# Optimization experiments

Measured on AMD Instinct MI355X. Metric: run time of the kernel, lower is better.

Reference implementation:

```python
import jax, jax.numpy as jnp
import numpy as np

B, T, E, H = 16, 4096, 64, 8
K, GADD, RADD, REGION = 256, 8, 8, 64
MIN_SIGMA, SIGMA_SCALE, SIGMA_BOOST = 0.05, 1.0, 2.0
VS = K * (4 + GADD + RADD)


def setup_inputs() -> dict:
    key = jax.random.key(0)
    ks = jax.random.split(key, 10)
    return {
        "x": jax.random.normal(ks[0], (B, T, E), jnp.float32),
        "Wq": jax.random.normal(ks[1], (E, E * H), jnp.float32) / np.float32(np.sqrt(E)),
        "Wk": jax.random.normal(ks[2], (E, E * H), jnp.float32) / np.float32(np.sqrt(E)),
        "Wv": jax.random.normal(ks[3], (E, E * H), jnp.float32) / np.float32(np.sqrt(E)),
        "Wu": jax.random.normal(ks[4], (H * E, E), jnp.float32) / np.float32(np.sqrt(H * E)),
        "bu": jnp.zeros((E,), jnp.float32),
        "means_p": jax.random.normal(ks[5], (K, 2), jnp.float32),
        "sigmas_p": jax.random.normal(ks[6], (K,), jnp.float32),
        "global_ints": jax.random.randint(ks[7], (B, 1, K, GADD, 2), 0, T, jnp.int32),
        "local_offsets": jax.random.randint(ks[8], (B, 1, K, RADD, 2), 0, REGION, jnp.int32),
    }


def _flip(x):
    # util.flip: sort each (i, j) pair so row >= col (below-diagonal / causal)
    hi = jnp.max(x, axis=-1, keepdims=True)
    lo = jnp.min(x, axis=-1, keepdims=True)
    return jnp.concatenate([hi, lo], axis=-1)


def _forward(x, Wq, Wk, Wv, Wu, bu, means_p, sigmas_p, global_ints, local_offsets):
    b, t, e = x.shape
    h, k = H, K

    # ---- hyper(): continuous means/sigmas over the (t, t) attention matrix
    means = jnp.broadcast_to(means_p[None, None], (b, 1, k, 2))
    means = _flip(means)
    means = jax.nn.sigmoid(means) * (t - 1)                       # (b,1,k,2) in [0, t-1]
    sig = jax.nn.softplus(sigmas_p + SIGMA_BOOST) + MIN_SIGMA     # (k,)
    sigmas = jnp.broadcast_to((sig * t * SIGMA_SCALE)[None, None, :, None], (b, 1, k, 2))

    # ---- ngenerate: 2^rank floor/ceil neighbours + global + relative-window samples
    fl, ce = jnp.floor(means), jnp.ceil(means)
    pat = jnp.array([[0., 0.], [0., 1.], [1., 0.], [1., 1.]], jnp.float32)  # (4,2)
    neigh = fl[:, :, :, None, :] * (1.0 - pat) + ce[:, :, :, None, :] * pat
    neigh = jnp.clip(neigh, 0, t - 1).astype(jnp.int32)           # (b,1,k,4,2)
    lower = jnp.clip(jnp.floor(means) - REGION // 2, 0, t - REGION).astype(jnp.int32)
    local = lower[:, :, :, None, :] + local_offsets               # (b,1,k,RADD,2)
    idx = jnp.concatenate([neigh, global_ints, local], axis=3).reshape(b, 1, VS, 2)
    idx = _flip(idx)                                              # (b,1,VS,2), row >= col

    # ---- densities: unnormalized Gaussian weight of each int tuple under each point
    indfl = idx.astype(jnp.float32)
    diff = (indfl[:, :, :, None, :] - means[:, :, None, :, :]) / sigmas[:, :, None, :, :]
    props = jnp.exp(-0.5 * jnp.sum(diff * diff, axis=-1))         # (b,1,VS,K)

    # ---- nduplicates: zero all-but-one of identical index tuples per batch
    ids = idx[:, 0, :, 0] * t + idx[:, 0, :, 1]                   # (b, VS)
    def dupmask(v):
        o = jnp.argsort(v)
        s = v[o]
        d = jnp.concatenate([jnp.zeros((1,), bool), s[1:] == s[:-1]])
        return jnp.zeros((VS,), bool).at[o].set(d)
    dups = jax.vmap(dupmask)(ids)                                  # (b, VS)
    props = jnp.where(dups[:, None, :, None], 0.0, props)
    props = props / jnp.sum(props, axis=2, keepdims=True)
    weights = jnp.sum(props, axis=3)                               # mvalues == 1 -> (b,1,VS)

    # ---- Q/K/V projections, per-head dim = e
    scale = e ** -0.25
    q = (x @ Wq).reshape(b, t, h, e).transpose(0, 2, 1, 3).reshape(b * h, t, e) * scale
    kk = (x @ Wk).reshape(b, t, h, e).transpose(0, 2, 1, 3).reshape(b * h, t, e) * scale
    v = (x @ Wv).reshape(b, t, h, e).transpose(0, 2, 1, 3).reshape(b * h, t, e)

    rows = jnp.broadcast_to(idx[:, 0, None, :, 0], (b, h, VS)).reshape(b * h, VS)
    cols = jnp.broadcast_to(idx[:, 0, None, :, 1], (b, h, VS)).reshape(b * h, VS)
    w = jnp.broadcast_to(weights[:, 0, None, :], (b, h, VS)).reshape(b * h, VS)

    sq = jnp.take_along_axis(q, rows[:, :, None], axis=1)          # (b*h, VS, e)
    sk = jnp.take_along_axis(kk, cols[:, :, None], axis=1)
    dot = w * jnp.sum(sq * sk, axis=-1)                            # (b*h, VS)

    # ---- segment (row-wise) softmax over the sparse pattern
    seg = (jnp.arange(b * h, dtype=jnp.int32)[:, None] * t + rows).reshape(-1)
    dflat = dot.reshape(-1)
    m = jax.lax.stop_gradient(jax.ops.segment_max(dflat, seg, num_segments=b * h * t))
    ex = jnp.exp(dflat - m[seg])
    ssum = jax.ops.segment_sum(ex, seg, num_segments=b * h * t)
    p = ex / ssum[seg]                                             # (b*h*VS,)

    # ---- sparse batched matmul: scatter-add p * V[col] into rows
    gathered = jnp.take_along_axis(v, cols[:, :, None], axis=1).reshape(-1, e)
    out = jax.ops.segment_sum(p[:, None] * gathered, seg, num_segments=b * h * t)
    out = out.reshape(b, h, t, e).transpose(0, 2, 1, 3).reshape(b, t, h * e)
    return out @ Wu + bu


def reference(x, Wq, Wk, Wv, Wu, bu, means_p, sigmas_p, global_ints, local_offsets):
    return _forward(x, Wq, Wk, Wv, Wu, bu, means_p, sigmas_p, global_ints, local_offsets)
```

## Files before the change

### kernel.cpp

```cpp
#include <hip/hip_runtime.h>
#include <hip/hip_bf16.h>
#include <math.h>

#define B 16
#define T 4096
#define E 64
#define H 8
#define KP 256
#define GADD 8
#define RADD 8
#define REGION 64
#define VS (KP * (4 + GADD + RADD))
#define NH (H * E)
#define NCHUNK 20
#define HSZ 16384

typedef __attribute__((ext_vector_type(8))) short bf16x8;
typedef __attribute__((ext_vector_type(4))) float f32x4;

__device__ inline ushort f2bf(float f) {
    union { __hip_bfloat16 h; ushort u; } cv;
    cv.h = __float2bfloat16(f);
    return cv.u;
}
__device__ inline float bflo(uint32_t p) { return __uint_as_float(p << 16); }
__device__ inline float bfhi(uint32_t p) { return __uint_as_float(p & 0xffff0000u); }
__device__ inline float sigm(float v) { return 1.f / (1.f + expf(-v)); }

__global__ void k_init(int* __restrict__ hkey, int* __restrict__ hval, int* __restrict__ chist) {
    int i = blockIdx.x * 256 + threadIdx.x;
    hkey[i] = -1;
    hval[i] = 0x7fffffff;
    #pragma unroll
    for (int j = 0; j < 5; ++j) chist[i + j * (B * HSZ)] = 0;
}

__global__ void k_prep_w(const float* __restrict__ Wq, const float* __restrict__ Wk,
                         const float* __restrict__ Wv, const float* __restrict__ Wu,
                         ushort* __restrict__ wfrag) {
    int t = blockIdx.x * 256 + threadIdx.x;
    if (t >= 3 * 32 * 2 * 64) return;
    int lane = t & 63, kf = (t >> 6) & 1, nf = (t >> 7) & 31, z = t >> 12;
    int col = nf * 16 + (lane & 15);
    int krow = kf * 32 + (lane >> 4) * 8;
    uint32_t v[8];
    if (z < 2) {
        const float* W = (z == 0) ? Wq : Wk;
        #pragma unroll
        for (int j = 0; j < 8; ++j) v[j] = f2bf(W[(size_t)(krow + j) * NH + col]);
    } else {
        int h = col >> 6, jc = col & 63;
        #pragma unroll
        for (int j = 0; j < 8; ++j) {
            const float* wvrow = Wv + (size_t)(krow + j) * NH + h * 64;
            const float* wucol = Wu + (size_t)h * 64 * 64 + jc;
            float acc = 0.f;
            for (int d = 0; d < 64; ++d) acc += wvrow[d] * wucol[d * 64];
            v[j] = f2bf(acc);
        }
    }
    uint4 r;
    r.x = v[0] | (v[1] << 16); r.y = v[2] | (v[3] << 16);
    r.z = v[4] | (v[5] << 16); r.w = v[6] | (v[7] << 16);
    *(uint4*)(wfrag + (size_t)t * 8) = r;
}

__global__ __launch_bounds__(256) void k_proj(const float* __restrict__ x,
        const ushort* __restrict__ wfrag,
        __hip_bfloat16* __restrict__ q, __hip_bfloat16* __restrict__ kk,
        __hip_bfloat16* __restrict__ vu) {
    int z = blockIdx.y;
    __hip_bfloat16* outp = (z == 0) ? q : (z == 1) ? kk : vu;
    int row0 = blockIdx.x * 64;
    int wv = threadIdx.x >> 6, lane = threadIdx.x & 63;
    int arow = lane & 15, akoff = (lane >> 4) * 8;

    bf16x8 bfr[8][2];
    #pragma unroll
    for (int nf = 0; nf < 8; ++nf) {
        size_t base = ((size_t)((z * 32 + wv * 8 + nf) * 2) * 64 + lane) * 8;
        bfr[nf][0] = *(const bf16x8*)(wfrag + base);
        bfr[nf][1] = *(const bf16x8*)(wfrag + base + 64 * 8);
    }

    #pragma unroll
    for (int mf = 0; mf < 4; ++mf) {
        const float* xp = x + (size_t)(row0 + mf * 16 + arow) * 64 + akoff;
        float4 fa0 = *(const float4*)xp;
        float4 fa1 = *(const float4*)(xp + 4);
        float4 fb0 = *(const float4*)(xp + 32);
        float4 fb1 = *(const float4*)(xp + 36);
        union { bf16x8 v; uint32_t u[4]; } ca, cb;
        ca.u[0] = (uint32_t)f2bf(fa0.x) | ((uint32_t)f2bf(fa0.y) << 16);
        ca.u[1] = (uint32_t)f2bf(fa0.z) | ((uint32_t)f2bf(fa0.w) << 16);
        ca.u[2] = (uint32_t)f2bf(fa1.x) | ((uint32_t)f2bf(fa1.y) << 16);
        ca.u[3] = (uint32_t)f2bf(fa1.z) | ((uint32_t)f2bf(fa1.w) << 16);
        cb.u[0] = (uint32_t)f2bf(fb0.x) | ((uint32_t)f2bf(fb0.y) << 16);
        cb.u[1] = (uint32_t)f2bf(fb0.z) | ((uint32_t)f2bf(fb0.w) << 16);
        cb.u[2] = (uint32_t)f2bf(fb1.x) | ((uint32_t)f2bf(fb1.y) << 16);
        cb.u[3] = (uint32_t)f2bf(fb1.z) | ((uint32_t)f2bf(fb1.w) << 16);
        bf16x8 a0 = ca.v, a1 = cb.v;
        f32x4 acc[8];
        #pragma unroll
        for (int nf = 0; nf < 8; ++nf) {
            f32x4 t = {0.f, 0.f, 0.f, 0.f};
            t = __builtin_amdgcn_mfma_f32_16x16x32_bf16(a0, bfr[nf][0], t, 0, 0, 0);
            t = __builtin_amdgcn_mfma_f32_16x16x32_bf16(a1, bfr[nf][1], t, 0, 0, 0);
            acc[nf] = t;
        }
        int rbase = row0 + mf * 16 + (lane >> 4) * 4;
        #pragma unroll
        for (int rg = 0; rg < 4; ++rg) {
            uint4 o;
            o.x = (uint32_t)f2bf(acc[0][rg]) | ((uint32_t)f2bf(acc[1][rg]) << 16);
            o.y = (uint32_t)f2bf(acc[2][rg]) | ((uint32_t)f2bf(acc[3][rg]) << 16);
            o.z = (uint32_t)f2bf(acc[4][rg]) | ((uint32_t)f2bf(acc[5][rg]) << 16);
            o.w = (uint32_t)f2bf(acc[6][rg]) | ((uint32_t)f2bf(acc[7][rg]) << 16);
            *(uint4*)((ushort*)outp + (size_t)(rbase + rg) * NH + wv * 128 + (lane & 15) * 8) = o;
        }
    }
}

__global__ void k_build_idx(const int* __restrict__ g_ints, const int* __restrict__ l_offs,
                            const float* __restrict__ means_p,
                            int* __restrict__ idxrow, int* __restrict__ idxcol,
                            int* __restrict__ hkey, int* __restrict__ hval) {
    int b = blockIdx.y;
    int s = blockIdx.x * 256 + threadIdx.x;
    int* keys = hkey + b * HSZ;
    int* vals = hval + b * HSZ;
    int k = s / 20, slot = s % 20;
    float pa = means_p[2 * k], pb = means_p[2 * k + 1];
    float m0 = sigm(fmaxf(pa, pb)) * (float)(T - 1);
    float m1 = sigm(fminf(pa, pb)) * (float)(T - 1);
    int i0, i1;
    if (slot < 4) {
        float a  = (slot & 2) ? ceilf(m0) : floorf(m0);
        float bb = (slot & 1) ? ceilf(m1) : floorf(m1);
        a  = fminf(fmaxf(a, 0.f), (float)(T - 1));
        bb = fminf(fmaxf(bb, 0.f), (float)(T - 1));
        i0 = (int)a; i1 = (int)bb;
    } else if (slot < 12) {
        const int* p = g_ints + ((size_t)((b * KP + k) * GADD) + (slot - 4)) * 2;
        i0 = p[0]; i1 = p[1];
    } else {
        int lo0 = (int)fminf(fmaxf(floorf(m0) - (float)(REGION / 2), 0.f), (float)(T - REGION));
        int lo1 = (int)fminf(fmaxf(floorf(m1) - (float)(REGION / 2), 0.f), (float)(T - REGION));
        const int* p = l_offs + ((size_t)((b * KP + k) * RADD) + (slot - 12)) * 2;
        i0 = lo0 + p[0]; i1 = lo1 + p[1];
    }
    int row = max(i0, i1), col = min(i0, i1);
    idxrow[b * VS + s] = row;
    idxcol[b * VS + s] = col;
    int id = row * T + col;
    unsigned h = ((unsigned)id * 2654435761u) >> 18;
    while (true) {
        int old = atomicCAS(&keys[h], -1, id);
        if (old == -1 || old == id) { atomicMin(&vals[h], s); break; }
        h = (h + 1) & (HSZ - 1);
    }
}

__global__ __launch_bounds__(256) void k_local(const int* __restrict__ idxrow,
        const int* __restrict__ idxcol, const int* __restrict__ hkey,
        const int* __restrict__ hval, int* __restrict__ lrank, int* __restrict__ dup,
        int* __restrict__ chist) {
    int b = blockIdx.y, chunk = blockIdx.x;
    int tid = threadIdx.x;
    int s = chunk * 256 + tid;
    int r = idxrow[b * VS + s];
    int c = idxcol[b * VS + s];
    __shared__ int srow[256];
    srow[tid] = r;
    __syncthreads();
    int lr = 0;
    #pragma unroll 8
    for (int t = 0; t < 256; ++t) {
        int rt = srow[t];
        lr += (t < tid && rt == r);
    }
    lrank[b * VS + s] = lr;
    atomicAdd(&chist[(size_t)(b * T + r) * NCHUNK + chunk], 1);
    const int* keys = hkey + b * HSZ;
    const int* vals = hval + b * HSZ;
    int id = r * T + c;
    unsigned h = ((unsigned)id * 2654435761u) >> 18;
    while (keys[h] != id) h = (h + 1) & (HSZ - 1);
    dup[b * VS + s] = (vals[h] != s);
}

__global__ void k_colsum(const int* __restrict__ idxrow, const int* __restrict__ idxcol,
                         const int* __restrict__ dup, const float* __restrict__ means_p,
                         const float* __restrict__ sigmas_p, float* __restrict__ colsum) {
    int k = blockIdx.x, b = blockIdx.y;
    float pa = means_p[2 * k], pb = means_p[2 * k + 1];
    float m0 = sigm(fmaxf(pa, pb)) * (float)(T - 1);
    float m1 = sigm(fminf(pa, pb)) * (float)(T - 1);
    float sp = sigmas_p[k] + 2.0f;
    float sg = (sp > 20.f) ? sp : log1pf(expf(sp));
    float inv = 1.f / ((sg + 0.05f) * (float)T);
    float acc = 0.f;
    for (int s = threadIdx.x; s < VS; s += 256) {
        if (!dup[b * VS + s]) {
            float d0 = ((float)idxrow[b * VS + s] - m0) * inv;
            float d1 = ((float)idxcol[b * VS + s] - m1) * inv;
            acc += __expf(-0.5f * (d0 * d0 + d1 * d1));
        }
    }
    __shared__ float red[256];
    red[threadIdx.x] = acc;
    __syncthreads();
    for (int o = 128; o > 0; o >>= 1) {
        if (threadIdx.x < o) red[threadIdx.x] += red[threadIdx.x + o];
        __syncthreads();
    }
    if (threadIdx.x == 0) colsum[b * KP + k] = red[0];
}

__global__ void k_weights(const int* __restrict__ idxrow, const int* __restrict__ idxcol,
                          const int* __restrict__ dup, const float* __restrict__ means_p,
                          const float* __restrict__ sigmas_p, const float* __restrict__ colsum,
                          float* __restrict__ wts) {
    int b = blockIdx.y;
    int s = blockIdx.x * 256 + threadIdx.x;
    __shared__ float sm[2 * KP], ss[KP], rc[KP];
    {
        int k = threadIdx.x;
        float pa = means_p[2 * k], pb = means_p[2 * k + 1];
        sm[2 * k]     = sigm(fmaxf(pa, pb)) * (float)(T - 1);
        sm[2 * k + 1] = sigm(fminf(pa, pb)) * (float)(T - 1);
        float sp = sigmas_p[k] + 2.0f;
        float sg = (sp > 20.f) ? sp : log1pf(expf(sp));
        ss[k] = 1.f / ((sg + 0.05f) * (float)T);
        rc[k] = 1.f / colsum[b * KP + k];
    }
    __syncthreads();
    float w = 0.f;
    if (!dup[b * VS + s]) {
        float r = (float)idxrow[b * VS + s], c = (float)idxcol[b * VS + s];
        #pragma unroll 4
        for (int k = 0; k < KP; ++k) {
            float d0 = (r - sm[2 * k]) * ss[k];
            float d1 = (c - sm[2 * k + 1]) * ss[k];
            w += __expf(-0.5f * (d0 * d0 + d1 * d1)) * rc[k];
        }
    }
    wts[b * VS + s] = w;
}

__global__ __launch_bounds__(1024) void k_scan(int* __restrict__ chist, int* __restrict__ rowptr) {
    int b = blockIdx.x, tid = threadIdx.x;
    __shared__ int part[1024];
    int v[4]; int loc = 0;
    #pragma unroll
    for (int j = 0; j < 4; ++j) {
        int row = tid * 4 + j;
        int* p = chist + (size_t)(b * T + row) * NCHUNK;
        int acc = 0;
        #pragma unroll
        for (int c = 0; c < NCHUNK; ++c) { int t = p[c]; p[c] = acc; acc += t; }
        v[j] = acc; loc += acc;
    }
    part[tid] = loc;
    __syncthreads();
    for (int off = 1; off < 1024; off <<= 1) {
        int t = (tid >= off) ? part[tid - off] : 0;
        __syncthreads();
        part[tid] += t;
        __syncthreads();
    }
    int excl = part[tid] - loc;
    #pragma unroll
    for (int j = 0; j < 4; ++j) { rowptr[b * (T + 1) + tid * 4 + j] = excl; excl += v[j]; }
    if (tid == 1023) rowptr[b * (T + 1) + T] = part[1023];
}

__global__ void k_scatter(const int* __restrict__ idxrow, const int* __restrict__ idxcol,
                          const float* __restrict__ wts, const int* __restrict__ lrank,
                          const int* __restrict__ chist, const int* __restrict__ rowptr,
                          int* __restrict__ scol, float* __restrict__ sw) {
    int b = blockIdx.y;
    int s = blockIdx.x * 256 + threadIdx.x;
    int r = idxrow[b * VS + s];
    int pos = rowptr[b * (T + 1) + r] + chist[(size_t)(b * T + r) * NCHUNK + (s >> 8)]
            + lrank[b * VS + s];
    scol[b * VS + pos] = idxcol[b * VS + s];
    sw[b * VS + pos] = wts[b * VS + s];
}

__global__ __launch_bounds__(256) void k_attn(
        const __hip_bfloat16* __restrict__ q, const __hip_bfloat16* __restrict__ kk,
        const __hip_bfloat16* __restrict__ vu, const int* __restrict__ rowptr,
        const int* __restrict__ scol, const float* __restrict__ sw,
        const float* __restrict__ bu, float* __restrict__ out) {
    int bid = blockIdx.x;
    int swz = ((bid & 7) << 11) | (bid >> 3);
    int gr = swz * 4 + (threadIdx.x >> 6);
    int b = gr >> 12;
    int r = gr & (T - 1);
    int lane = threadIdx.x & 63;
    int p0 = rowptr[b * (T + 1) + r], p1 = rowptr[b * (T + 1) + r + 1];

    uint4 q4 = *(const uint4*)((const ushort*)q + (size_t)gr * NH + lane * 8);
    float qv[8] = { bflo(q4.x), bfhi(q4.x), bflo(q4.y), bfhi(q4.y),
                    bflo(q4.z), bfhi(q4.z), bflo(q4.w), bfhi(q4.w) };

    float m0 = -INFINITY, s0 = 0.f, m1 = -INFINITY, s1 = 0.f;
    float av[8] = {0.f,0.f,0.f,0.f,0.f,0.f,0.f,0.f};

    for (int e = p0; e < p1; ++e) {
        int c = scol[b * VS + e];
        float w = sw[b * VS + e];
        size_t off = ((size_t)(b * T + c)) * NH + lane * 8;
        uint4 k4 = *(const uint4*)((const ushort*)kk + off);
        float dp0 = qv[0]*bflo(k4.x) + qv[1]*bfhi(k4.x) + qv[2]*bflo(k4.y) + qv[3]*bfhi(k4.y);
        float dp1 = qv[4]*bflo(k4.z) + qv[5]*bfhi(k4.z) + qv[6]*bflo(k4.w) + qv[7]*bfhi(k4.w);
        dp0 += __shfl_xor(dp0, 1);
        dp0 += __shfl_xor(dp0, 2);
        dp0 += __shfl_xor(dp0, 4);
        dp0 += __shfl_xor(dp0, 8);
        dp1 += __shfl_xor(dp1, 1);
        dp1 += __shfl_xor(dp1, 2);
        dp1 += __shfl_xor(dp1, 4);
        dp1 += __shfl_xor(dp1, 8);
        float d0 = 0.125f * w * dp0;
        float d1 = 0.125f * w * dp1;
        uint4 v4 = *(const uint4*)((const ushort*)vu + off);
        float vf[8] = { bflo(v4.x), bfhi(v4.x), bflo(v4.y), bfhi(v4.y),
                        bflo(v4.z), bfhi(v4.z), bflo(v4.w), bfhi(v4.w) };
        float nm0 = fmaxf(m0, d0), c0 = __expf(m0 - nm0), t0 = __expf(d0 - nm0);
        float nm1 = fmaxf(m1, d1), c1 = __expf(m1 - nm1), t1 = __expf(d1 - nm1);
        s0 = s0 * c0 + t0; m0 = nm0;
        s1 = s1 * c1 + t1; m1 = nm1;
        #pragma unroll
        for (int u = 0; u < 4; ++u) av[u] = av[u] * c0 + t0 * vf[u];
        #pragma unroll
        for (int u = 4; u < 8; ++u) av[u] = av[u] * c1 + t1 * vf[u];
    }

    float i0 = (p1 > p0) ? (1.f / s0) : 0.f;
    float i1 = (p1 > p0) ? (1.f / s1) : 0.f;
    float res[4];
    #pragma unroll
    for (int u = 0; u < 4; ++u) {
        float v = av[u] * i0 + av[u + 4] * i1;
        v += __shfl_xor(v, 16);
        v += __shfl_xor(v, 32);
        res[u] = v;
    }
    if (lane < 16) {
        #pragma unroll
        for (int u = 0; u < 4; ++u)
            out[(size_t)gr * E + u * 16 + lane] = res[u] + bu[u * 16 + lane];
    }
}

extern "C" void kernel_launch(void* const* d_in, const int* in_sizes, int n_in,
                              void* d_out, int out_size, void* d_ws, size_t ws_size,
                              hipStream_t stream) {
    const float* x        = (const float*)d_in[0];
    const float* Wq       = (const float*)d_in[1];
    const float* Wk       = (const float*)d_in[2];
    const float* Wv       = (const float*)d_in[3];
    const float* Wu       = (const float*)d_in[4];
    const float* bu       = (const float*)d_in[5];
    const float* means_p  = (const float*)d_in[6];
    const float* sigmas_p = (const float*)d_in[7];
    const int*   g_ints   = (const int*)d_in[8];
    const int*   l_offs   = (const int*)d_in[9];
    float* out = (float*)d_out;

    char* ws = (char*)d_ws;
    size_t o = 0;
    auto alloc = [&](size_t bytes) -> void* {
        void* p = ws + o;
        o += (bytes + 255) & ~(size_t)255;
        return p;
    };
    __hip_bfloat16* q   = (__hip_bfloat16*)alloc((size_t)B * T * NH * 2);
    __hip_bfloat16* kk  = (__hip_bfloat16*)alloc((size_t)B * T * NH * 2);
    __hip_bfloat16* vu  = (__hip_bfloat16*)alloc((size_t)B * T * NH * 2);
    ushort* wfrag = (ushort*)alloc((size_t)3 * 32 * 2 * 64 * 8 * 2);
    int*   idxrow = (int*)alloc((size_t)B * VS * 4);
    int*   idxcol = (int*)alloc((size_t)B * VS * 4);
    float* wts    = (float*)alloc((size_t)B * VS * 4);
    int*   lrank  = (int*)alloc((size_t)B * VS * 4);
    int*   dup    = (int*)alloc((size_t)B * VS * 4);
    float* colsum = (float*)alloc((size_t)B * KP * 4);
    int*   rowptr = (int*)alloc((size_t)B * (T + 1) * 4);
    int*   scol   = (int*)alloc((size_t)B * VS * 4);
    float* sw     = (float*)alloc((size_t)B * VS * 4);
    int*   hkey   = (int*)alloc((size_t)B * HSZ * 4);
    int*   hval   = (int*)alloc((size_t)B * HSZ * 4);
    int*   chist  = (int*)alloc((size_t)B * T * NCHUNK * 4);

    k_init<<<B * HSZ / 256, 256, 0, stream>>>(hkey, hval, chist);
    k_prep_w<<<(3 * 32 * 2 * 64 + 255) / 256, 256, 0, stream>>>(Wq, Wk, Wv, Wu, wfrag);
    k_build_idx<<<dim3(VS / 256, B), 256, 0, stream>>>(g_ints, l_offs, means_p, idxrow, idxcol, hkey, hval);
    k_local<<<dim3(NCHUNK, B), 256, 0, stream>>>(idxrow, idxcol, hkey, hval, lrank, dup, chist);
    k_colsum<<<dim3(KP, B), 256, 0, stream>>>(idxrow, idxcol, dup, means_p, sigmas_p, colsum);
    k_weights<<<dim3(VS / 256, B), 256, 0, stream>>>(idxrow, idxcol, dup, means_p, sigmas_p, colsum, wts);
    k_scan<<<B, 1024, 0, stream>>>(chist, rowptr);
    k_scatter<<<dim3(VS / 256, B), 256, 0, stream>>>(idxrow, idxcol, wts, lrank, chist, rowptr, scol, sw);
    k_proj<<<dim3(B * T / 64, 3), 256, 0, stream>>>(x, wfrag, q, kk, vu);
    k_attn<<<B * T / 4, 256, 0, stream>>>(q, kk, vu, rowptr, scol, sw, bu, out);
}
```

Measured before the change: 200.8 us.

## Skip projection stores for unused rows/cols and early-exit empty attention rows

Marks which key/value columns are referenced by the sparse pattern and has the projection kernel write Q only for rows that have entries and K/VU only for referenced columns, cutting the large bf16 store traffic. The attention kernel now exits early for empty rows by writing only the bias, and the block swizzle is removed. The fp32-to-bf16 conversion of x moves into a separate pre-pass kernel, which adds a launch and an extra buffer round trip. Validity rests on unused rows never being read.

Result: slower. 212.3 us (+5.7%).

```diff
diff --git a/kernel.cpp b/kernel.cpp
--- a/kernel.cpp
+++ b/kernel.cpp
@@ -27,12 +27,26 @@
 __device__ inline float bfhi(uint32_t p) { return __uint_as_float(p & 0xffff0000u); }
 __device__ inline float sigm(float v) { return 1.f / (1.f + expf(-v)); }
 
-__global__ void k_init(int* __restrict__ hkey, int* __restrict__ hval, int* __restrict__ chist) {
+__global__ void k_init(int* __restrict__ hkey, int* __restrict__ hval,
+                       int* __restrict__ chist, int* __restrict__ colneed) {
     int i = blockIdx.x * 256 + threadIdx.x;
     hkey[i] = -1;
     hval[i] = 0x7fffffff;
     #pragma unroll
     for (int j = 0; j < 5; ++j) chist[i + j * (B * HSZ)] = 0;
+    if (i < B * T) colneed[i] = 0;
+}
+
+__global__ void k_prep_x(const float* __restrict__ x, ushort* __restrict__ xb) {
+    int i = (blockIdx.x * 256 + threadIdx.x) * 8;
+    float4 a = *(const float4*)(x + i);
+    float4 b = *(const float4*)(x + i + 4);
+    uint4 r;
+    r.x = (uint32_t)f2bf(a.x) | ((uint32_t)f2bf(a.y) << 16);
+    r.y = (uint32_t)f2bf(a.z) | ((uint32_t)f2bf(a.w) << 16);
+    r.z = (uint32_t)f2bf(b.x) | ((uint32_t)f2bf(b.y) << 16);
+    r.w = (uint32_t)f2bf(b.z) | ((uint32_t)f2bf(b.w) << 16);
+    *(uint4*)(xb + i) = r;
 }
 
 __global__ void k_prep_w(const float* __restrict__ Wq, const float* __restrict__ Wk,
@@ -65,8 +79,9 @@
     *(uint4*)(wfrag + (size_t)t * 8) = r;
 }
 
-__global__ __launch_bounds__(256) void k_proj(const float* __restrict__ x,
-        const ushort* __restrict__ wfrag,
+__global__ __launch_bounds__(256) void k_proj(const ushort* __restrict__ xb,
+        const ushort* __restrict__ wfrag, const int* __restrict__ rowptr,
+        const int* __restrict__ colneed,
         __hip_bfloat16* __restrict__ q, __hip_bfloat16* __restrict__ kk,
         __hip_bfloat16* __restrict__ vu) {
     int z = blockIdx.y;
@@ -85,21 +100,8 @@
 
     #pragma unroll
     for (int mf = 0; mf < 4; ++mf) {
-        const float* xp = x + (size_t)(row0 + mf * 16 + arow) * 64 + akoff;
-        float4 fa0 = *(const float4*)xp;
-        float4 fa1 = *(const float4*)(xp + 4);
-        float4 fb0 = *(const float4*)(xp + 32);
-        float4 fb1 = *(const float4*)(xp + 36);
-        union { bf16x8 v; uint32_t u[4]; } ca, cb;
-        ca.u[0] = (uint32_t)f2bf(fa0.x) | ((uint32_t)f2bf(fa0.y) << 16);
-        ca.u[1] = (uint32_t)f2bf(fa0.z) | ((uint32_t)f2bf(fa0.w) << 16);
-        ca.u[2] = (uint32_t)f2bf(fa1.x) | ((uint32_t)f2bf(fa1.y) << 16);
-        ca.u[3] = (uint32_t)f2bf(fa1.z) | ((uint32_t)f2bf(fa1.w) << 16);
-        cb.u[0] = (uint32_t)f2bf(fb0.x) | ((uint32_t)f2bf(fb0.y) << 16);
-        cb.u[1] = (uint32_t)f2bf(fb0.z) | ((uint32_t)f2bf(fb0.w) << 16);
-        cb.u[2] = (uint32_t)f2bf(fb1.x) | ((uint32_t)f2bf(fb1.y) << 16);
-        cb.u[3] = (uint32_t)f2bf(fb1.z) | ((uint32_t)f2bf(fb1.w) << 16);
-        bf16x8 a0 = ca.v, a1 = cb.v;
+        bf16x8 a0 = *(const bf16x8*)(xb + (size_t)(row0 + mf * 16 + arow) * 64 + akoff);
+        bf16x8 a1 = *(const bf16x8*)(xb + (size_t)(row0 + mf * 16 + arow) * 64 + 32 + akoff);
         f32x4 acc[8];
         #pragma unroll
         for (int nf = 0; nf < 8; ++nf) {
@@ -111,12 +113,22 @@
         int rbase = row0 + mf * 16 + (lane >> 4) * 4;
         #pragma unroll
         for (int rg = 0; rg < 4; ++rg) {
-            uint4 o;
-            o.x = (uint32_t)f2bf(acc[0][rg]) | ((uint32_t)f2bf(acc[1][rg]) << 16);
-            o.y = (uint32_t)f2bf(acc[2][rg]) | ((uint32_t)f2bf(acc[3][rg]) << 16);
-            o.z = (uint32_t)f2bf(acc[4][rg]) | ((uint32_t)f2bf(acc[5][rg]) << 16);
-            o.w = (uint32_t)f2bf(acc[6][rg]) | ((uint32_t)f2bf(acc[7][rg]) << 16);
-            *(uint4*)((ushort*)outp + (size_t)(rbase + rg) * NH + wv * 128 + (lane & 15) * 8) = o;
+            int grow = rbase + rg;
+            int need;
+            if (z == 0) {
+                int bb = grow >> 12, rr = grow & (T - 1);
+                need = rowptr[bb * (T + 1) + rr + 1] - rowptr[bb * (T + 1) + rr];
+            } else {
+                need = colneed[grow];
+            }
+            if (need) {
+                uint4 o;
+                o.x = (uint32_t)f2bf(acc[0][rg]) | ((uint32_t)f2bf(acc[1][rg]) << 16);
+                o.y = (uint32_t)f2bf(acc[2][rg]) | ((uint32_t)f2bf(acc[3][rg]) << 16);
+                o.z = (uint32_t)f2bf(acc[4][rg]) | ((uint32_t)f2bf(acc[5][rg]) << 16);
+                o.w = (uint32_t)f2bf(acc[6][rg]) | ((uint32_t)f2bf(acc[7][rg]) << 16);
+                *(uint4*)((ushort*)outp + (size_t)grow * NH + wv * 128 + (lane & 15) * 8) = o;
+            }
         }
     }
 }
@@ -124,7 +136,8 @@
 __global__ void k_build_idx(const int* __restrict__ g_ints, const int* __restrict__ l_offs,
                             const float* __restrict__ means_p,
                             int* __restrict__ idxrow, int* __restrict__ idxcol,
-                            int* __restrict__ hkey, int* __restrict__ hval) {
+                            int* __restrict__ hkey, int* __restrict__ hval,
+                            int* __restrict__ colneed) {
     int b = blockIdx.y;
     int s = blockIdx.x * 256 + threadIdx.x;
     int* keys = hkey + b * HSZ;
@@ -152,6 +165,7 @@
     int row = max(i0, i1), col = min(i0, i1);
     idxrow[b * VS + s] = row;
     idxcol[b * VS + s] = col;
+    colneed[b * T + col] = 1;
     int id = row * T + col;
     unsigned h = ((unsigned)id * 2654435761u) >> 18;
     while (true) {
@@ -293,13 +307,20 @@
         const __hip_bfloat16* __restrict__ vu, const int* __restrict__ rowptr,
         const int* __restrict__ scol, const float* __restrict__ sw,
         const float* __restrict__ bu, float* __restrict__ out) {
-    int bid = blockIdx.x;
-    int swz = ((bid & 7) << 11) | (bid >> 3);
-    int gr = swz * 4 + (threadIdx.x >> 6);
+    int gr = blockIdx.x * 4 + (threadIdx.x >> 6);
     int b = gr >> 12;
     int r = gr & (T - 1);
     int lane = threadIdx.x & 63;
     int p0 = rowptr[b * (T + 1) + r], p1 = rowptr[b * (T + 1) + r + 1];
+
+    if (p0 == p1) {
+        if (lane < 16) {
+            #pragma unroll
+            for (int u = 0; u < 4; ++u)
+                out[(size_t)gr * E + u * 16 + lane] = bu[u * 16 + lane];
+        }
+        return;
+    }
 
     uint4 q4 = *(const uint4*)((const ushort*)q + (size_t)gr * NH + lane * 8);
     float qv[8] = { bflo(q4.x), bfhi(q4.x), bflo(q4.y), bfhi(q4.y),
@@ -338,8 +359,8 @@
         for (int u = 4; u < 8; ++u) av[u] = av[u] * c1 + t1 * vf[u];
     }
 
-    float i0 = (p1 > p0) ? (1.f / s0) : 0.f;
-    float i1 = (p1 > p0) ? (1.f / s1) : 0.f;
+    float i0 = 1.f / s0;
+    float i1 = 1.f / s1;
     float res[4];
     #pragma unroll
     for (int u = 0; u < 4; ++u) {
@@ -380,6 +401,7 @@
     __hip_bfloat16* q   = (__hip_bfloat16*)alloc((size_t)B * T * NH * 2);
     __hip_bfloat16* kk  = (__hip_bfloat16*)alloc((size_t)B * T * NH * 2);
     __hip_bfloat16* vu  = (__hip_bfloat16*)alloc((size_t)B * T * NH * 2);
+    ushort* xb    = (ushort*)alloc((size_t)B * T * E * 2);
     ushort* wfrag = (ushort*)alloc((size_t)3 * 32 * 2 * 64 * 8 * 2);
     int*   idxrow = (int*)alloc((size_t)B * VS * 4);
     int*   idxcol = (int*)alloc((size_t)B * VS * 4);
@@ -393,15 +415,17 @@
     int*   hkey   = (int*)alloc((size_t)B * HSZ * 4);
     int*   hval   = (int*)alloc((size_t)B * HSZ * 4);
     int*   chist  = (int*)alloc((size_t)B * T * NCHUNK * 4);
-
-    k_init<<<B * HSZ / 256, 256, 0, stream>>>(hkey, hval, chist);
+    int*   colneed= (int*)alloc((size_t)B * T * 4);
+
+    k_init<<<B * HSZ / 256, 256, 0, stream>>>(hkey, hval, chist, colneed);
+    k_prep_x<<<(B * T * E / 8) / 256, 256, 0, stream>>>(x, xb);
     k_prep_w<<<(3 * 32 * 2 * 64 + 255) / 256, 256, 0, stream>>>(Wq, Wk, Wv, Wu, wfrag);
-    k_build_idx<<<dim3(VS / 256, B), 256, 0, stream>>>(g_ints, l_offs, means_p, idxrow, idxcol, hkey, hval);
+    k_build_idx<<<dim3(VS / 256, B), 256, 0, stream>>>(g_ints, l_offs, means_p, idxrow, idxcol, hkey, hval, colneed);
     k_local<<<dim3(NCHUNK, B), 256, 0, stream>>>(idxrow, idxcol, hkey, hval, lrank, dup, chist);
     k_colsum<<<dim3(KP, B), 256, 0, stream>>>(idxrow, idxcol, dup, means_p, sigmas_p, colsum);
     k_weights<<<dim3(VS / 256, B), 256, 0, stream>>>(idxrow, idxcol, dup, means_p, sigmas_p, colsum, wts);
     k_scan<<<B, 1024, 0, stream>>>(chist, rowptr);
     k_scatter<<<dim3(VS / 256, B), 256, 0, stream>>>(idxrow, idxcol, wts, lrank, chist, rowptr, scol, sw);
-    k_proj<<<dim3(B * T / 64, 3), 256, 0, stream>>>(x, wfrag, q, kk, vu);
+    k_proj<<<dim3(B * T / 64, 3), 256, 0, stream>>>(xb, wfrag, rowptr, colneed, q, kk, vu);
     k_attn<<<B * T / 4, 256, 0, stream>>>(q, kk, vu, rowptr, scol, sw, bu, out);
 }
```
